# Optimization experiments

Measured on AMD Instinct MI355X. Metric: run time of the kernel, lower is better.

Reference implementation:

```python
import jax, jax.numpy as jnp
import numpy as np

DIM, HEADS, WS, MLP_RATIO = 384, 8, 8, 2.0
HID = int(DIM * MLP_RATIO)
EPS = 1e-5


def layernorm(x, w, b):
    mu = jnp.mean(x, axis=-1, keepdims=True)
    var = jnp.mean(jnp.square(x - mu), axis=-1, keepdims=True)
    return (x - mu) * jax.lax.rsqrt(var + EPS) * w + b


def setup_inputs() -> dict:
    key = jax.random.key(0)
    ks = jax.random.split(key, 8)
    s = 0.02
    return {
        "x": jax.random.normal(ks[0], (8, DIM, 128, 128), dtype=jnp.float32),
        "n1_w": jnp.ones((DIM,), jnp.float32),
        "n1_b": jnp.zeros((DIM,), jnp.float32),
        "in_w": jax.random.normal(ks[1], (3 * DIM, DIM), jnp.float32) * s,  # qkv packed, Linear convention
        "in_b": jnp.zeros((3 * DIM,), jnp.float32),
        "out_w": jax.random.normal(ks[2], (DIM, DIM), jnp.float32) * s,
        "out_b": jnp.zeros((DIM,), jnp.float32),
        "n2_w": jnp.ones((DIM,), jnp.float32),
        "n2_b": jnp.zeros((DIM,), jnp.float32),
        "w1": jax.random.normal(ks[3], (HID, DIM), jnp.float32) * s,
        "b1": jnp.zeros((HID,), jnp.float32),
        "w2": jax.random.normal(ks[4], (DIM, HID), jnp.float32) * s,
        "b2": jnp.zeros((DIM,), jnp.float32),
    }


def _block(x, n1_w, n1_b, in_w, in_b, out_w, out_b, n2_w, n2_b, w1, b1, w2, b2):
    b, c, h, w = x.shape
    ph = (WS - h % WS) % WS
    pw = (WS - w % WS) % WS
    if ph or pw:
        x = jnp.pad(x, ((0, 0), (0, 0), (0, ph), (0, pw)))
    hp, wp = x.shape[2], x.shape[3]
    nh, nw = hp // WS, wp // WS
    # window partition: [b,c,hp,wp] -> [b*nh*nw, WS*WS, c]
    win = x.reshape(b, c, nh, WS, nw, WS).transpose(0, 2, 4, 3, 5, 1).reshape(-1, WS * WS, c)

    y = layernorm(win, n1_w, n1_b)
    # packed qkv projection
    qkv = jnp.einsum('nsc,fc->nsf', y, in_w) + in_b  # [N, S, 3C]
    q, k, v = jnp.split(qkv, 3, axis=-1)
    hd = c // HEADS
    def split_heads(t):
        return t.reshape(t.shape[0], t.shape[1], HEADS, hd)
    q, k, v = split_heads(q), split_heads(k), split_heads(v)
    scale = 1.0 / np.sqrt(hd).astype(np.float32)
    att = jnp.einsum('nqhd,nkhd->nhqk', q * scale, k)
    att = jax.nn.softmax(att, axis=-1)
    o = jnp.einsum('nhqk,nkhd->nqhd', att, v).reshape(-1, WS * WS, c)
    o = jnp.einsum('nsc,fc->nsf', o, out_w) + out_b
    win = win + o

    y = layernorm(win, n2_w, n2_b)
    y = jax.nn.gelu(jnp.einsum('nsc,fc->nsf', y, w1) + b1, approximate=False)
    win = win + jnp.einsum('nsf,cf->nsc', y, w2) + b2

    # window reverse
    xo = win.reshape(b, nh, nw, WS, WS, c).transpose(0, 5, 1, 3, 2, 4).reshape(b, c, hp, wp)
    return xo[:, :, :h, :w]


def reference(x, n1_w, n1_b, in_w, in_b, out_w, out_b, n2_w, n2_b, w1, b1, w2, b2):
    return _block(x, n1_w, n1_b, in_w, in_b, out_w, out_b, n2_w, n2_b, w1, b1, w2, b2)
```

## Files before the change

kernel.cpp:

```cpp
#include <hip/hip_runtime.h>

#define NWIN 2048
#define TPB 256

typedef __attribute__((ext_vector_type(8))) short short8;
typedef __attribute__((ext_vector_type(4))) float floatx4;

__device__ __forceinline__ float bf2f(unsigned short u) {
    union { unsigned int i; float f; } v; v.i = ((unsigned int)u) << 16; return v.f;
}
__device__ __forceinline__ unsigned short f2bf(float f) {
    union { float f; unsigned int i; } v; v.f = f;
    unsigned int u = v.i;
    return (unsigned short)((u + 0x7FFFu + ((u >> 16) & 1u)) >> 16);
}
__device__ __forceinline__ floatx4 mfma16(short8 a, short8 b, floatx4 c) {
    return __builtin_amdgcn_mfma_f32_16x16x32_bf16(a, b, c, 0, 0, 0);
}

__global__ __launch_bounds__(TPB) void k0_cvt(
    const float* __restrict__ inw, const float* __restrict__ inb,
    const float* __restrict__ outw, const float* __restrict__ outb,
    const float* __restrict__ n1w, const float* __restrict__ n1b,
    const float* __restrict__ n2w, const float* __restrict__ n2b,
    const float* __restrict__ w1, const float* __restrict__ b1,
    const float* __restrict__ w2, const float* __restrict__ b2,
    unsigned short* __restrict__ dst)
{
    int i = blockIdx.x * TPB + threadIdx.x;
    if (i >= 1183872) return;
    const float* src; int off;
    if      (i < 442368)  { src = inw;  off = 0; }
    else if (i < 443520)  { src = inb;  off = 442368; }
    else if (i < 590976)  { src = outw; off = 443520; }
    else if (i < 591360)  { src = outb; off = 590976; }
    else if (i < 591744)  { src = n1w;  off = 591360; }
    else if (i < 592128)  { src = n1b;  off = 591744; }
    else if (i < 592512)  { src = n2w;  off = 592128; }
    else if (i < 592896)  { src = n2b;  off = 592512; }
    else if (i < 887808)  { src = w1;   off = 592896; }
    else if (i < 888576)  { src = b1;   off = 887808; }
    else if (i < 1183488) { src = w2;   off = 888576; }
    else                  { src = b2;   off = 1183488; }
    dst[i] = f2bf(src[i - off]);
}

__global__ __launch_bounds__(512) void k2_attn(
    const float* __restrict__ x,
    unsigned short* __restrict__ yo,
    const unsigned short* __restrict__ n1w,
    const unsigned short* __restrict__ n1b,
    const unsigned short* __restrict__ in_w,
    const unsigned short* __restrict__ in_b,
    const unsigned short* __restrict__ out_w,
    const unsigned short* __restrict__ out_b)
{
    __shared__ __align__(16) unsigned short ylds[24576];
    __shared__ __align__(16) unsigned short wbuf[8][6144];
    const int tid = threadIdx.x;
    const int h = tid >> 6, lane = tid & 63;
    const int l15 = lane & 15, lg = lane >> 4;
    const int widx = blockIdx.x;
    const int b = widx >> 8, nh = (widx >> 4) & 15, nw = widx & 15;
    const size_t base = (size_t)widx * 24576;
    const size_t xbase = (size_t)b * 384 * 16384 + (size_t)nh * 8 * 128 + (size_t)nw * 8;
    const short8 z8 = {0, 0, 0, 0, 0, 0, 0, 0};

    unsigned short* bufA = &wbuf[h][0];
    unsigned short* bufB = &wbuf[h][3072];

    for (int idx = tid; idx < 6144; idx += 512) {
        int c = idx >> 4, i = (idx >> 1) & 7, half = idx & 1;
        floatx4 v = *(const floatx4*)(x + xbase + (size_t)c * 16384 + i * 128 + half * 4);
        #pragma unroll
        for (int j = 0; j < 4; ++j) {
            int m = i * 8 + half * 4 + j;
            ylds[m * 384 + (((c >> 3) ^ (m & 7)) << 3) + (c & 7)] = f2bf(v[j]);
        }
    }
    __syncthreads();

    {
        int row = tid >> 3, part = tid & 7;
        float s = 0.f, sq = 0.f;
        #pragma unroll
        for (int g = 0; g < 6; ++g) {
            int ck = part * 6 + g;
            short8 v = *(const short8*)&ylds[row * 384 + ((ck ^ (row & 7)) << 3)];
            #pragma unroll
            for (int j = 0; j < 8; ++j) { float f = bf2f((unsigned short)v[j]); s += f; sq += f * f; }
        }
        s += __shfl_xor(s, 1); s += __shfl_xor(s, 2); s += __shfl_xor(s, 4);
        sq += __shfl_xor(sq, 1); sq += __shfl_xor(sq, 2); sq += __shfl_xor(sq, 4);
        float mu = s * (1.f / 384.f);
        float rs = rsqrtf(sq * (1.f / 384.f) - mu * mu + 1e-5f);
        #pragma unroll
        for (int g = 0; g < 6; ++g) {
            int ck = part * 6 + g;
            unsigned short* p = &ylds[row * 384 + ((ck ^ (row & 7)) << 3)];
            short8 v = *(const short8*)p;
            short8 wv = *(const short8*)(n1w + ck * 8);
            short8 bv = *(const short8*)(n1b + ck * 8);
            short8 o;
            #pragma unroll
            for (int j = 0; j < 8; ++j)
                o[j] = (short)f2bf((bf2f((unsigned short)v[j]) - mu) * rs *
                                   bf2f((unsigned short)wv[j]) + bf2f((unsigned short)bv[j]));
            *(short8*)p = o;
        }
    }
    __syncthreads();

    const float scale = 0.14433756729740643f;
    const unsigned short* wq = in_w + (size_t)(h * 48) * 384;
    const unsigned short* wk = in_w + (size_t)(384 + h * 48) * 384;
    const unsigned short* wv = in_w + (size_t)(768 + h * 48) * 384;

    {
        floatx4 acc[4][6];
        #pragma unroll
        for (int mt = 0; mt < 4; ++mt)
            #pragma unroll
            for (int i = 0; i < 6; ++i) acc[mt][i] = (floatx4){0, 0, 0, 0};
        #pragma unroll 1
        for (int ks = 0; ks < 12; ++ks) {
            short8 a[4];
            #pragma unroll
            for (int mt = 0; mt < 4; ++mt) {
                int m = mt * 16 + l15;
                a[mt] = *(const short8*)&ylds[m * 384 + (((ks * 4 + lg) ^ (m & 7)) << 3)];
            }
            #pragma unroll
            for (int nt = 0; nt < 3; ++nt) {
                short8 bq = *(const short8*)(wq + (size_t)(nt * 16 + l15) * 384 + ks * 32 + lg * 8);
                #pragma unroll
                for (int mt = 0; mt < 4; ++mt) acc[mt][nt] = mfma16(a[mt], bq, acc[mt][nt]);
                short8 bk = *(const short8*)(wk + (size_t)(nt * 16 + l15) * 384 + ks * 32 + lg * 8);
                #pragma unroll
                for (int mt = 0; mt < 4; ++mt) acc[mt][3 + nt] = mfma16(a[mt], bk, acc[mt][3 + nt]);
            }
        }
        #pragma unroll
        for (int sel = 0; sel < 2; ++sel) {
            unsigned short* dst = sel ? bufB : bufA;
            #pragma unroll
            for (int nt = 0; nt < 3; ++nt) {
                int d = nt * 16 + l15;
                int g = d >> 3;
                float bias = bf2f(in_b[sel * 384 + h * 48 + d]);
                #pragma unroll
                for (int mt = 0; mt < 4; ++mt)
                    #pragma unroll
                    for (int r = 0; r < 4; ++r) {
                        int mm = mt * 16 + lg * 4 + r;
                        dst[mm * 48 + ((g ^ (mm & 1)) << 3) + (d & 7)] =
                            f2bf(acc[mt][sel * 3 + nt][r] + bias);
                    }
            }
        }
    }

    floatx4 sacc[4][4];
    #pragma unroll
    for (int mt = 0; mt < 4; ++mt)
        #pragma unroll
        for (int nt = 0; nt < 4; ++nt) sacc[mt][nt] = (floatx4){0, 0, 0, 0};
    {
        short8 b0[4], b1[4];
        #pragma unroll
        for (int nt = 0; nt < 4; ++nt) {
            int n = nt * 16 + l15;
            b0[nt] = *(const short8*)&bufB[n * 48 + ((lg ^ (n & 1)) << 3)];
            b1[nt] = (lg < 2) ? *(const short8*)&bufB[n * 48 + (((4 + lg) ^ (n & 1)) << 3)] : z8;
        }
        #pragma unroll
        for (int mt = 0; mt < 4; ++mt) {
            int mq = mt * 16 + l15;
            short8 a0 = *(const short8*)&bufA[mq * 48 + ((lg ^ (mq & 1)) << 3)];
            #pragma unroll
            for (int nt = 0; nt < 4; ++nt) sacc[mt][nt] = mfma16(a0, b0[nt], sacc[mt][nt]);
            short8 a1 = (lg < 2) ? *(const short8*)&bufA[mq * 48 + (((4 + lg) ^ (mq & 1)) << 3)] : z8;
            #pragma unroll
            for (int nt = 0; nt < 4; ++nt) sacc[mt][nt] = mfma16(a1, b1[nt], sacc[mt][nt]);
        }
    }

    #pragma unroll
    for (int mt = 0; mt < 4; ++mt)
        #pragma unroll
        for (int r = 0; r < 4; ++r) {
            float mx = fmaxf(fmaxf(sacc[mt][0][r], sacc[mt][1][r]),
                             fmaxf(sacc[mt][2][r], sacc[mt][3][r]));
            mx = fmaxf(mx, __shfl_xor(mx, 1));
            mx = fmaxf(mx, __shfl_xor(mx, 2));
            mx = fmaxf(mx, __shfl_xor(mx, 4));
            mx = fmaxf(mx, __shfl_xor(mx, 8));
            float e[4];
            #pragma unroll
            for (int nt = 0; nt < 4; ++nt) e[nt] = __expf(scale * (sacc[mt][nt][r] - mx));
            float sm = e[0] + e[1] + e[2] + e[3];
            sm += __shfl_xor(sm, 1); sm += __shfl_xor(sm, 2);
            sm += __shfl_xor(sm, 4); sm += __shfl_xor(sm, 8);
            float inv = 1.f / sm;
            #pragma unroll
            for (int nt = 0; nt < 4; ++nt) sacc[mt][nt][r] = e[nt] * inv;
        }

    #pragma unroll
    for (int mt = 0; mt < 4; ++mt)
        #pragma unroll
        for (int r = 0; r < 4; ++r) {
            int row = mt * 16 + lg * 4 + r;
            #pragma unroll
            for (int ntl = 0; ntl < 2; ++ntl) {
                int lc = ntl * 16 + l15;
                bufA[row * 32 + (((lc >> 3) ^ (row & 3)) << 3) + (lc & 7)] =
                    f2bf(sacc[mt][ntl][r]);
            }
        }

    floatx4 vacc[4][3];
    #pragma unroll
    for (int mt = 0; mt < 4; ++mt)
        #pragma unroll
        for (int nt = 0; nt < 3; ++nt) vacc[mt][nt] = (floatx4){0, 0, 0, 0};
    #pragma unroll 1
    for (int ks = 0; ks < 12; ++ks) {
        short8 a[4];
        #pragma unroll
        for (int mt = 0; mt < 4; ++mt) {
            int m = mt * 16 + l15;
            a[mt] = *(const short8*)&ylds[m * 384 + (((ks * 4 + lg) ^ (m & 7)) << 3)];
        }
        #pragma unroll
        for (int nt = 0; nt < 3; ++nt) {
            short8 bv = *(const short8*)(wv + (size_t)(nt * 16 + l15) * 384 + ks * 32 + lg * 8);
            #pragma unroll
            for (int mt = 0; mt < 4; ++mt) vacc[mt][nt] = mfma16(a[mt], bv, vacc[mt][nt]);
        }
    }
    #pragma unroll
    for (int nt = 0; nt < 3; ++nt) {
        int d = nt * 16 + l15;
        float bias = bf2f(in_b[768 + h * 48 + d]);
        #pragma unroll
        for (int mt = 0; mt < 4; ++mt)
            #pragma unroll
            for (int r = 0; r < 4; ++r) {
                int t = mt * 16 + lg * 4 + r;
                bufB[d * 64 + (((t >> 3) ^ (d & 7)) << 3) + (t & 7)] =
                    f2bf(vacc[mt][nt][r] + bias);
            }
    }

    floatx4 oacc[4][3];
    #pragma unroll
    for (int mt = 0; mt < 4; ++mt)
        #pragma unroll
        for (int nt = 0; nt < 3; ++nt) oacc[mt][nt] = (floatx4){0, 0, 0, 0};
    #pragma unroll
    for (int kh = 0; kh < 2; ++kh) {
        if (kh == 1) {
            #pragma unroll
            for (int mt = 0; mt < 4; ++mt)
                #pragma unroll
                for (int r = 0; r < 4; ++r) {
                    int row = mt * 16 + lg * 4 + r;
                    #pragma unroll
                    for (int ntl = 0; ntl < 2; ++ntl) {
                        int lc = ntl * 16 + l15;
                        bufA[row * 32 + (((lc >> 3) ^ (row & 3)) << 3) + (lc & 7)] =
                            f2bf(sacc[mt][2 + ntl][r]);
                    }
                }
        }
        #pragma unroll
        for (int mt = 0; mt < 4; ++mt) {
            int m = mt * 16 + l15;
            short8 a = *(const short8*)&bufA[m * 32 + ((lg ^ (m & 3)) << 3)];
            #pragma unroll
            for (int nt = 0; nt < 3; ++nt) {
                int d = nt * 16 + l15;
                int tg = kh * 4 + lg;
                short8 bb = *(const short8*)&bufB[d * 64 + ((tg ^ (d & 7)) << 3)];
                oacc[mt][nt] = mfma16(a, bb, oacc[mt][nt]);
            }
        }
    }
    #pragma unroll
    for (int nt = 0; nt < 3; ++nt)
        #pragma unroll
        for (int mt = 0; mt < 4; ++mt)
            #pragma unroll
            for (int r = 0; r < 4; ++r) {
                int mm = mt * 16 + lg * 4 + r;
                int d = nt * 16 + l15;
                bufA[mm * 48 + (((d >> 3) ^ (mm & 1)) << 3) + (d & 7)] =
                    f2bf(oacc[mt][nt][r]);
            }
    __syncthreads();

    {
        floatx4 acc[3][4];
        #pragma unroll
        for (int nt = 0; nt < 3; ++nt)
            #pragma unroll
            for (int mt = 0; mt < 4; ++mt) acc[nt][mt] = (floatx4){0, 0, 0, 0};
        #pragma unroll 1
        for (int ks = 0; ks < 12; ++ks) {
            int col8 = ks * 4 + lg;
            int hh = (col8 * 43) >> 8;
            int lc = col8 - hh * 6;
            short8 a[4];
            #pragma unroll
            for (int mt = 0; mt < 4; ++mt) {
                int m = mt * 16 + l15;
                a[mt] = *(const short8*)&wbuf[hh][m * 48 + ((lc ^ (m & 1)) << 3)];
            }
            #pragma unroll
            for (int nt = 0; nt < 3; ++nt) {
                int f = h * 48 + nt * 16 + l15;
                short8 bb = *(const short8*)(out_w + (size_t)f * 384 + ks * 32 + lg * 8);
                #pragma unroll
                for (int mt = 0; mt < 4; ++mt)
                    acc[nt][mt] = mfma16(a[mt], bb, acc[nt][mt]);
            }
        }
        #pragma unroll
        for (int nt = 0; nt < 3; ++nt) {
            int col = h * 48 + nt * 16 + l15;
            float bias = bf2f(out_b[col]);
            #pragma unroll
            for (int mt = 0; mt < 4; ++mt) {
                #pragma unroll
                for (int r = 0; r < 4; ++r) {
                    int m = mt * 16 + lg * 4 + r;
                    int i = m >> 3, j = m & 7;
                    float res = x[xbase + (size_t)col * 16384 + i * 128 + j];
                    yo[base + (size_t)m * 384 + col] = f2bf(acc[nt][mt][r] + bias + res);
                }
            }
        }
    }
}

__global__ __launch_bounds__(512, 4) void k4_mlp(
    unsigned short* __restrict__ wbuf,
    const unsigned short* __restrict__ n2w,
    const unsigned short* __restrict__ n2b,
    const unsigned short* __restrict__ w1,
    const unsigned short* __restrict__ b1,
    const unsigned short* __restrict__ w2,
    const unsigned short* __restrict__ b2)
{
    __shared__ __align__(16) unsigned short ylds[24576];
    __shared__ __align__(16) unsigned short hch[16384];
    const int tid = threadIdx.x;
    const int wave = tid >> 6, lane = tid & 63;
    const int l15 = lane & 15, lg = lane >> 4;
    const int widx = blockIdx.x;
    const size_t base = (size_t)widx * 24576;

    {
        int row = tid >> 3, part = tid & 7;
        const unsigned short* src = wbuf + base + row * 384 + part * 48;
        float s = 0.f, sq = 0.f;
        #pragma unroll
        for (int g = 0; g < 6; ++g) {
            short8 v = *(const short8*)(src + g * 8);
            #pragma unroll
            for (int j = 0; j < 8; ++j) { float f = bf2f((unsigned short)v[j]); s += f; sq += f * f; }
        }
        s += __shfl_xor(s, 1); s += __shfl_xor(s, 2); s += __shfl_xor(s, 4);
        sq += __shfl_xor(sq, 1); sq += __shfl_xor(sq, 2); sq += __shfl_xor(sq, 4);
        float mu = s * (1.f / 384.f);
        float rs = rsqrtf(sq * (1.f / 384.f) - mu * mu + 1e-5f);
        #pragma unroll
        for (int g = 0; g < 6; ++g) {
            int ck = part * 6 + g;
            short8 v = *(const short8*)(src + g * 8);
            short8 wv = *(const short8*)(n2w + ck * 8);
            short8 bv = *(const short8*)(n2b + ck * 8);
            short8 o;
            #pragma unroll
            for (int j = 0; j < 8; ++j)
                o[j] = (short)f2bf((bf2f((unsigned short)v[j]) - mu) * rs *
                                   bf2f((unsigned short)wv[j]) + bf2f((unsigned short)bv[j]));
            *(short8*)&ylds[row * 384 + ((ck ^ (row & 7)) << 3)] = o;
        }
    }
    __syncthreads();

    floatx4 acc2[12];
    #pragma unroll
    for (int i = 0; i < 12; ++i) acc2[i] = (floatx4){0, 0, 0, 0};

    #pragma unroll 1
    for (int cc = 0; cc < 3; ++cc) {
        floatx4 acc[8];
        #pragma unroll
        for (int i = 0; i < 8; ++i) acc[i] = (floatx4){0, 0, 0, 0};
        #pragma unroll 1
        for (int ks = 0; ks < 12; ++ks) {
            short8 a[4];
            #pragma unroll
            for (int mt = 0; mt < 4; ++mt) {
                int m = mt * 16 + l15;
                a[mt] = *(const short8*)&ylds[m * 384 + (((ks * 4 + lg) ^ (m & 7)) << 3)];
            }
            #pragma unroll
            for (int nt = 0; nt < 2; ++nt) {
                int f = cc * 256 + wave * 32 + nt * 16 + l15;
                short8 bb = *(const short8*)(w1 + (size_t)f * 384 + ks * 32 + lg * 8);
                #pragma unroll
                for (int mt = 0; mt < 4; ++mt)
                    acc[nt * 4 + mt] = mfma16(a[mt], bb, acc[nt * 4 + mt]);
            }
        }
        #pragma unroll
        for (int nt = 0; nt < 2; ++nt) {
            int dloc = wave * 32 + nt * 16 + l15;
            float bias = bf2f(b1[cc * 256 + dloc]);
            #pragma unroll
            for (int mt = 0; mt < 4; ++mt) {
                #pragma unroll
                for (int r = 0; r < 4; ++r) {
                    int t = mt * 16 + lg * 4 + r;
                    float v = acc[nt * 4 + mt][r] + bias;
                    float g = 0.5f * v * (1.f + erff(v * 0.70710678118654752f));
                    hch[t * 256 + (((dloc >> 3) ^ (t & 7)) << 3) + (dloc & 7)] = f2bf(g);
                }
            }
        }
        __syncthreads();
        #pragma unroll 1
        for (int ks = 0; ks < 8; ++ks) {
            short8 a[4];
            #pragma unroll
            for (int mt = 0; mt < 4; ++mt) {
                int m = mt * 16 + l15;
                a[mt] = *(const short8*)&hch[m * 256 + (((ks * 4 + lg) ^ (m & 7)) << 3)];
            }
            #pragma unroll
            for (int nt = 0; nt < 3; ++nt) {
                int c = wave * 48 + nt * 16 + l15;
                short8 bb = *(const short8*)(w2 + (size_t)c * 768 + cc * 256 + ks * 32 + lg * 8);
                #pragma unroll
                for (int mt = 0; mt < 4; ++mt)
                    acc2[nt * 4 + mt] = mfma16(a[mt], bb, acc2[nt * 4 + mt]);
            }
        }
        __syncthreads();
    }

    #pragma unroll
    for (int nt = 0; nt < 3; ++nt) {
        int col = wave * 48 + nt * 16 + l15;
        float bias = bf2f(b2[col]);
        #pragma unroll
        for (int mt = 0; mt < 4; ++mt) {
            #pragma unroll
            for (int r = 0; r < 4; ++r) {
                int mm = mt * 16 + lg * 4 + r;
                float res = bf2f(wbuf[base + (size_t)mm * 384 + col]);
                wbuf[base + (size_t)mm * 384 + col] = f2bf(acc2[nt * 4 + mt][r] + bias + res);
            }
        }
    }
}

__global__ __launch_bounds__(TPB) void k5_out(
    const unsigned short* __restrict__ res,
    float* __restrict__ out)
{
    __shared__ __align__(16) unsigned short t[128][200];
    const int tid = threadIdx.x;
    const int bid = blockIdx.x;
    const int ch = bid & 1, i = (bid >> 1) & 7, nh = (bid >> 4) & 15, b = bid >> 8;

    {
        int wrow = tid >> 1, half = tid & 1;
        int nw = wrow >> 3, j = wrow & 7;
        size_t rbase = (size_t)(((b * 16 + nh) * 16) + nw) * 24576 + (i * 8 + j) * 384 + ch * 192;
        #pragma unroll
        for (int g = 0; g < 12; ++g) {
            int cc = half * 12 + g;
            short8 v = *(const short8*)(res + rbase + cc * 8);
            *(short8*)&t[wrow][cc * 8] = v;
        }
    }
    __syncthreads();
    {
        int q = tid >> 5, wg = tid & 31;
        int w0 = wg * 4;
        size_t obase = ((size_t)b * 384 + ch * 192) * 16384 + (size_t)(nh * 8 + i) * 128 + w0;
        #pragma unroll 1
        for (int cc = 0; cc < 24; ++cc) {
            int cp = cc * 8 + q;
            floatx4 v;
            #pragma unroll
            for (int k = 0; k < 4; ++k) v[k] = bf2f(t[w0 + k][cp]);
            *(floatx4*)(out + obase + (size_t)cp * 16384) = v;
        }
    }
}

extern "C" void kernel_launch(void* const* d_in, const int* in_sizes, int n_in,
                              void* d_out, int out_size, void* d_ws, size_t ws_size,
                              hipStream_t stream) {
    (void)in_sizes; (void)n_in; (void)out_size; (void)ws_size;
    const float* x    = (const float*)d_in[0];
    const float* n1w  = (const float*)d_in[1];
    const float* n1b  = (const float*)d_in[2];
    const float* inw  = (const float*)d_in[3];
    const float* inb  = (const float*)d_in[4];
    const float* outw = (const float*)d_in[5];
    const float* outb = (const float*)d_in[6];
    const float* n2w  = (const float*)d_in[7];
    const float* n2b  = (const float*)d_in[8];
    const float* w1   = (const float*)d_in[9];
    const float* b1   = (const float*)d_in[10];
    const float* w2   = (const float*)d_in[11];
    const float* b2   = (const float*)d_in[12];
    unsigned short* wsu  = (unsigned short*)d_ws;
    unsigned short* ybuf = wsu;
    unsigned short* wb   = wsu + 50331648;
    const unsigned short* inw_b  = wb;
    const unsigned short* inb_b  = wb + 442368;
    const unsigned short* outw_b = wb + 443520;
    const unsigned short* outb_b = wb + 590976;
    const unsigned short* n1w_b  = wb + 591360;
    const unsigned short* n1b_b  = wb + 591744;
    const unsigned short* n2w_b  = wb + 592128;
    const unsigned short* n2b_b  = wb + 592512;
    const unsigned short* w1_b   = wb + 592896;
    const unsigned short* b1_b   = wb + 887808;
    const unsigned short* w2_b   = wb + 888576;
    const unsigned short* b2_b   = wb + 1183488;
    float* out = (float*)d_out;

    k0_cvt<<<dim3((1183872 + TPB - 1) / TPB), dim3(TPB), 0, stream>>>(
        inw, inb, outw, outb, n1w, n1b, n2w, n2b, w1, b1, w2, b2, wb);
    k2_attn<<<dim3(NWIN), dim3(512), 0, stream>>>(
        x, ybuf, n1w_b, n1b_b, inw_b, inb_b, outw_b, outb_b);
    k4_mlp<<<dim3(NWIN), dim3(512), 0, stream>>>(ybuf, n2w_b, n2b_b, w1_b, b1_b, w2_b, b2_b);
    k5_out<<<dim3(NWIN), dim3(TPB), 0, stream>>>(ybuf, out);
}
```

Measured before the change: 1.323 ms.

## Fuse V projection into QK GEMM loop and store V in reused LDS

The V projection is now computed in the same K loop as Q and K, so each A tile read from LDS feeds nine accumulator tiles instead of being reloaded in a separate pass. V is written transposed into a per-head slice of the LN buffer after a barrier, which frees bufB. Launch bounds now request two blocks per CU and several GEMM loops are unrolled by two. The larger accumulator set (36 floatx4) and the occupancy target together raise register pressure and may cause spills.

```diff
diff --git a/kernel.cpp b/kernel.cpp
--- a/kernel.cpp
+++ b/kernel.cpp
@@ -45,7 +45,7 @@
     dst[i] = f2bf(src[i - off]);
 }
 
-__global__ __launch_bounds__(512) void k2_attn(
+__global__ __launch_bounds__(512, 2) void k2_attn(
     const float* __restrict__ x,
     unsigned short* __restrict__ yo,
     const unsigned short* __restrict__ n1w,
@@ -68,6 +68,7 @@
 
     unsigned short* bufA = &wbuf[h][0];
     unsigned short* bufB = &wbuf[h][3072];
+    unsigned short* vt   = &ylds[h * 3072];
 
     for (int idx = tid; idx < 6144; idx += 512) {
         int c = idx >> 4, i = (idx >> 1) & 7, half = idx & 1;
@@ -114,15 +115,15 @@
     const float scale = 0.14433756729740643f;
     const unsigned short* wq = in_w + (size_t)(h * 48) * 384;
     const unsigned short* wk = in_w + (size_t)(384 + h * 48) * 384;
-    const unsigned short* wv = in_w + (size_t)(768 + h * 48) * 384;
-
-    {
-        floatx4 acc[4][6];
+    const unsigned short* wvp = in_w + (size_t)(768 + h * 48) * 384;
+
+    {
+        floatx4 acc[4][9];
         #pragma unroll
         for (int mt = 0; mt < 4; ++mt)
             #pragma unroll
-            for (int i = 0; i < 6; ++i) acc[mt][i] = (floatx4){0, 0, 0, 0};
-        #pragma unroll 1
+            for (int i = 0; i < 9; ++i) acc[mt][i] = (floatx4){0, 0, 0, 0};
+        #pragma unroll 2
         for (int ks = 0; ks < 12; ++ks) {
             short8 a[4];
             #pragma unroll
@@ -138,6 +139,9 @@
                 short8 bk = *(const short8*)(wk + (size_t)(nt * 16 + l15) * 384 + ks * 32 + lg * 8);
                 #pragma unroll
                 for (int mt = 0; mt < 4; ++mt) acc[mt][3 + nt] = mfma16(a[mt], bk, acc[mt][3 + nt]);
+                short8 bv = *(const short8*)(wvp + (size_t)(nt * 16 + l15) * 384 + ks * 32 + lg * 8);
+                #pragma unroll
+                for (int mt = 0; mt < 4; ++mt) acc[mt][6 + nt] = mfma16(a[mt], bv, acc[mt][6 + nt]);
             }
         }
         #pragma unroll
@@ -157,6 +161,20 @@
                             f2bf(acc[mt][sel * 3 + nt][r] + bias);
                     }
             }
+        }
+        __syncthreads();
+        #pragma unroll
+        for (int nt = 0; nt < 3; ++nt) {
+            int d = nt * 16 + l15;
+            float bias = bf2f(in_b[768 + h * 48 + d]);
+            #pragma unroll
+            for (int mt = 0; mt < 4; ++mt)
+                #pragma unroll
+                for (int r = 0; r < 4; ++r) {
+                    int t = mt * 16 + lg * 4 + r;
+                    vt[d * 64 + (((t >> 3) ^ (d & 7)) << 3) + (t & 7)] =
+                        f2bf(acc[mt][6 + nt][r] + bias);
+                }
         }
     }
 
@@ -218,40 +236,6 @@
                     f2bf(sacc[mt][ntl][r]);
             }
         }
-
-    floatx4 vacc[4][3];
-    #pragma unroll
-    for (int mt = 0; mt < 4; ++mt)
-        #pragma unroll
-        for (int nt = 0; nt < 3; ++nt) vacc[mt][nt] = (floatx4){0, 0, 0, 0};
-    #pragma unroll 1
-    for (int ks = 0; ks < 12; ++ks) {
-        short8 a[4];
-        #pragma unroll
-        for (int mt = 0; mt < 4; ++mt) {
-            int m = mt * 16 + l15;
-            a[mt] = *(const short8*)&ylds[m * 384 + (((ks * 4 + lg) ^ (m & 7)) << 3)];
-        }
-        #pragma unroll
-        for (int nt = 0; nt < 3; ++nt) {
-            short8 bv = *(const short8*)(wv + (size_t)(nt * 16 + l15) * 384 + ks * 32 + lg * 8);
-            #pragma unroll
-            for (int mt = 0; mt < 4; ++mt) vacc[mt][nt] = mfma16(a[mt], bv, vacc[mt][nt]);
-        }
-    }
-    #pragma unroll
-    for (int nt = 0; nt < 3; ++nt) {
-        int d = nt * 16 + l15;
-        float bias = bf2f(in_b[768 + h * 48 + d]);
-        #pragma unroll
-        for (int mt = 0; mt < 4; ++mt)
-            #pragma unroll
-            for (int r = 0; r < 4; ++r) {
-                int t = mt * 16 + lg * 4 + r;
-                bufB[d * 64 + (((t >> 3) ^ (d & 7)) << 3) + (t & 7)] =
-                    f2bf(vacc[mt][nt][r] + bias);
-            }
-    }
 
     floatx4 oacc[4][3];
     #pragma unroll
@@ -282,7 +266,7 @@
             for (int nt = 0; nt < 3; ++nt) {
                 int d = nt * 16 + l15;
                 int tg = kh * 4 + lg;
-                short8 bb = *(const short8*)&bufB[d * 64 + ((tg ^ (d & 7)) << 3)];
+                short8 bb = *(const short8*)&vt[d * 64 + ((tg ^ (d & 7)) << 3)];
                 oacc[mt][nt] = mfma16(a, bb, oacc[mt][nt]);
             }
         }
@@ -306,7 +290,7 @@
         for (int nt = 0; nt < 3; ++nt)
             #pragma unroll
             for (int mt = 0; mt < 4; ++mt) acc[nt][mt] = (floatx4){0, 0, 0, 0};
-        #pragma unroll 1
+        #pragma unroll 2
         for (int ks = 0; ks < 12; ++ks) {
             int col8 = ks * 4 + lg;
             int hh = (col8 * 43) >> 8;
@@ -400,7 +384,7 @@
         floatx4 acc[8];
         #pragma unroll
         for (int i = 0; i < 8; ++i) acc[i] = (floatx4){0, 0, 0, 0};
-        #pragma unroll 1
+        #pragma unroll 2
         for (int ks = 0; ks < 12; ++ks) {
             short8 a[4];
             #pragma unroll
@@ -433,7 +417,7 @@
             }
         }
         __syncthreads();
-        #pragma unroll 1
+        #pragma unroll 2
         for (int ks = 0; ks < 8; ++ks) {
             short8 a[4];
             #pragma unroll
```

New measurement: 1.359 ms. 1.03x slower.
